# Optimization experiments

Hardware: AMD Instinct MI355X
Metric: run time of the kernel (lower is better)

Reference implementation:

```python
import jax, jax.numpy as jnp
import numpy as np

K = 3        # kernel_size
PAD = 1      # padding ('same' for stride 1)
RANK = 53    # CP rank from compression=10: round(27*32*64/(10*(9+32+64)))


def _kaiming_uniform(key, shape, fan_in):
    # matches nn.init.kaiming_uniform_(a=sqrt(5)): bound = 1/sqrt(fan_in)
    bound = 1.0 / np.sqrt(fan_in)
    return jax.random.uniform(key, shape, jnp.float32, -bound, bound)


def setup_inputs() -> dict:
    key = jax.random.key(0)
    ks = jax.random.split(key, 7)
    B, Cin, Cout, H, W, D = 1, 32, 64, 56, 56, 56
    x = jax.random.normal(ks[0], (B, Cin, H, W, D), jnp.float32)
    # CP factor matrices (fan_in = second dim for torch's 2D kaiming)
    U_kh = _kaiming_uniform(ks[1], (K, RANK), RANK)
    U_kw = _kaiming_uniform(ks[2], (K, RANK), RANK)
    U_kd = _kaiming_uniform(ks[3], (K, RANK), RANK)
    U_cin = _kaiming_uniform(ks[4], (Cin, RANK), RANK)
    U_cout = _kaiming_uniform(ks[5], (RANK, Cout), Cout)
    bias = jax.random.normal(ks[6], (Cout,), jnp.float32)
    return {"x": x, "U_kh": U_kh, "U_kw": U_kw, "U_kd": U_kd,
            "U_cin": U_cin, "U_cout": U_cout, "bias": bias}


def reference(x, U_kh, U_kw, U_kd, U_cin, U_cout, bias):
    B, C, H, W, D = x.shape
    xp = jnp.pad(x, ((0, 0), (0, 0), (PAD, PAD), (PAD, PAD), (PAD, PAD)))
    # im2col patches: patches[i,j,l,b,c,x,y,z] = xp[b,c,x+i,y+j,z+l]
    # (same values/ordering as torch unfold(2).unfold(3).unfold(4), stride=1)
    patches = jnp.stack([
        xp[:, :, i:i + H, j:j + W, l:l + D]
        for i in range(K) for j in range(K) for l in range(K)
    ]).reshape(K, K, K, B, C, H, W, D)
    # CP tensor-network contraction (legs: k_h,k_w,k_d,c_in share rank r -> c_out)
    out = jnp.einsum('ijlbcxyz,ir,jr,lr,cr,ro->boxyz',
                     patches, U_kh, U_kw, U_kd, U_cin, U_cout,
                     optimize=True)
    return out + bias[None, :, None, None, None]
```

## Files before the change

### kernel.cpp

```cpp
#include <hip/hip_runtime.h>


#define NP 175616
#define NQ 43904
#define HSTR 3136
#define QH 784
#define CIN 32
#define RK 53
#define COUT 64
#define SCR 53

__global__ __launch_bounds__(256) void k0_t(const float* __restrict__ Ucin,
                                            float* __restrict__ Ut)
{
    int t = blockIdx.x * 256 + threadIdx.x;
    if (t < RK * CIN) {
        int r = t >> 5, c = t & 31;
        Ut[t] = Ucin[c * RK + r];
    }
}

__global__ __launch_bounds__(256) void k1n(
    const float* __restrict__ x, const float* __restrict__ Ut,
    float* __restrict__ T1)
{
    const int p = blockIdx.x * 256 + threadIdx.x;
    float xv[CIN];
#pragma unroll
    for (int c = 0; c < CIN; ++c) xv[c] = x[c * NP + p];
#pragma unroll 2
    for (int r = 0; r < RK; ++r) {
        const float* U = Ut + r * CIN;
        float acc = 0.f;
#pragma unroll
        for (int c = 0; c < CIN; ++c) acc += xv[c] * U[c];
        T1[(size_t)r * NP + p] = acc;
    }
}

__global__ __launch_bounds__(256) void k2n(
    float* T1, const float* __restrict__ Ukw, const float* __restrict__ Ukd)
{
    __shared__ float sIn[3136];
    __shared__ float sA[3136];
    const int h = blockIdx.x;
    const int r = blockIdx.y;
    const int tid = threadIdx.x;
    const float kd0 = Ukd[r], kd1 = Ukd[RK + r], kd2 = Ukd[2 * RK + r];
    const float kw0 = Ukw[r], kw1 = Ukw[RK + r], kw2 = Ukw[2 * RK + r];
    float4* P4 = (float4*)(T1 + (size_t)r * NP + h * HSTR);

    for (int i = tid; i < QH; i += 256)
        ((float4*)sIn)[i] = P4[i];
    __syncthreads();

    for (int i = tid; i < QH; i += 256) {
        int w = i / 14, d0 = (i - w * 14) * 4;
        const float* b = &sIn[w * 56 + d0];
        float4 c = *(const float4*)b;
        float lm = (d0 > 0)  ? b[-1] : 0.f;
        float rp = (d0 < 52) ? b[4]  : 0.f;
        float4 o;
        o.x = lm  * kd0 + c.x * kd1 + c.y * kd2;
        o.y = c.x * kd0 + c.y * kd1 + c.z * kd2;
        o.z = c.y * kd0 + c.z * kd1 + c.w * kd2;
        o.w = c.z * kd0 + c.w * kd1 + rp  * kd2;
        ((float4*)sA)[i] = o;
    }
    __syncthreads();

    for (int i = tid; i < QH; i += 256) {
        int w = i / 14;
        float4 m = ((const float4*)sA)[i];
        float4 a0, a2;
        a0.x = a0.y = a0.z = a0.w = 0.f; a2 = a0;
        if (w > 0)  a0 = ((const float4*)sA)[i - 14];
        if (w < 55) a2 = ((const float4*)sA)[i + 14];
        float4 res;
        res.x = a0.x * kw0 + m.x * kw1 + a2.x * kw2;
        res.y = a0.y * kw0 + m.y * kw1 + a2.y * kw2;
        res.z = a0.z * kw0 + m.z * kw1 + a2.z * kw2;
        res.w = a0.w * kw0 + m.w * kw1 + a2.w * kw2;
        P4[i] = res;
    }
}

__global__ __launch_bounds__(256, 4) void k3n(
    const float4* __restrict__ Ta, const float* __restrict__ Ucout,
    const float* __restrict__ bias, const float* __restrict__ Ukh,
    float4* __restrict__ Out)
{
    const int lane = threadIdx.x & 63;
    int og = (threadIdx.x >> 6) << 4;
    og = __builtin_amdgcn_readfirstlane(og);
    const int q = blockIdx.x * 64 + lane;
    const int h = q / QH;
    const bool hm = (h > 0), hp = (h < 55);

    float4 a[16];
#pragma unroll
    for (int o = 0; o < 16; ++o) {
        float b = bias[og + o];
        a[o].x = b; a[o].y = b; a[o].z = b; a[o].w = b;
    }
#pragma unroll 2
    for (int r = 0; r < RK; ++r) {
        const float4* S = Ta + (size_t)r * NQ + q;
        const float k0 = Ukh[r], k1 = Ukh[RK + r], k2 = Ukh[2 * RK + r];
        float4 B = S[0];
        float4 A; A.x = 0.f; A.y = 0.f; A.z = 0.f; A.w = 0.f;
        float4 C = A;
        if (hm) A = S[-QH];
        if (hp) C = S[QH];
        float4 t;
        t.x = A.x * k0 + B.x * k1 + C.x * k2;
        t.y = A.y * k0 + B.y * k1 + C.y * k2;
        t.z = A.z * k0 + B.z * k1 + C.z * k2;
        t.w = A.w * k0 + B.w * k1 + C.w * k2;
        const float* Ur = Ucout + r * COUT + og;
#pragma unroll
        for (int o = 0; o < 16; ++o) {
            float u = Ur[o];
            a[o].x += t.x * u; a[o].y += t.y * u;
            a[o].z += t.z * u; a[o].w += t.w * u;
        }
    }
#pragma unroll
    for (int o = 0; o < 16; ++o)
        Out[(size_t)(og + o) * NQ + q] = a[o];
}


__global__ __launch_bounds__(256) void k1_chunk(
    const float* __restrict__ x, const float* __restrict__ Ucin,
    float* T, int r0, int nr)
{
    __shared__ float sU[11 * CIN];
    const int tid = threadIdx.x;
    for (int t = tid; t < nr * CIN; t += 256) {
        int lr = t >> 5, c = t & 31;
        sU[t] = Ucin[c * RK + (r0 + lr)];
    }
    __syncthreads();
    const int p = blockIdx.x * 256 + tid;
    float xv[CIN];
#pragma unroll
    for (int c = 0; c < CIN; ++c) xv[c] = x[c * NP + p];
#pragma unroll 1
    for (int lr = 0; lr < nr; ++lr) {
        float acc = 0.f;
#pragma unroll
        for (int c = 0; c < CIN; ++c) acc += xv[c] * sU[lr * CIN + c];
        T[(size_t)(SCR + lr) * NP + p] = acc;
    }
}

__global__ __launch_bounds__(256) void k2_chunk(
    const float* __restrict__ Ukh, const float* __restrict__ Ukw,
    const float* __restrict__ Ukd, float* T, int r0)
{
    __shared__ float sIn[5800];
    __shared__ float sA[5600];
    const int lr = blockIdx.z;
    const int r  = r0 + lr;
    const int h0 = blockIdx.x * 8, w0 = blockIdx.y * 8;
    const int tid = threadIdx.x;
    const float kh0 = Ukh[r], kh1 = Ukh[RK + r], kh2 = Ukh[2 * RK + r];
    const float kw0 = Ukw[r], kw1 = Ukw[RK + r], kw2 = Ukw[2 * RK + r];
    const float kd0 = Ukd[r], kd1 = Ukd[RK + r], kd2 = Ukd[2 * RK + r];
    const float* T1r = T + (size_t)(SCR + lr) * NP;

    for (int idx = tid; idx < 5800; idx += 256) {
        int d = idx % 58; int t2 = idx / 58; int ww = t2 % 10; int hh = t2 / 10;
        int gh = h0 + hh - 1, gw = w0 + ww - 1, gd = d - 1;
        float v = 0.f;
        if ((unsigned)gh < 56u && (unsigned)gw < 56u && (unsigned)gd < 56u)
            v = T1r[gh * HSTR + gw * 56 + gd];
        sIn[idx] = v;
    }
    __syncthreads();
    for (int idx = tid; idx < 5600; idx += 256) {
        int d = idx % 56; int t2 = idx / 56; int ww = t2 % 10; int hh = t2 / 10;
        const float* b = &sIn[(hh * 10 + ww) * 58 + d];
        sA[idx] = b[0] * kd0 + b[1] * kd1 + b[2] * kd2;
    }
    __syncthreads();
    const float k00 = kh0 * kw0, k01 = kh0 * kw1, k02 = kh0 * kw2;
    const float k10 = kh1 * kw0, k11 = kh1 * kw1, k12 = kh1 * kw2;
    const float k20 = kh2 * kw0, k21 = kh2 * kw1, k22 = kh2 * kw2;
    for (int idx = tid; idx < 3584; idx += 256) {
        int d = idx % 56; int t2 = idx / 56; int ww = t2 % 8; int hh = t2 / 8;
        const float* a = &sA[(hh * 10 + ww) * 56 + d];
        float acc = a[0]    * k00 + a[56]   * k01 + a[112]  * k02
                  + a[560]  * k10 + a[616]  * k11 + a[672]  * k12
                  + a[1120] * k20 + a[1176] * k21 + a[1232] * k22;
        T[(size_t)r * NP + (h0 + hh) * HSTR + (w0 + ww) * 56 + d] = acc;
    }
}

__global__ __launch_bounds__(256) void k3_out(
    float* T, const float* __restrict__ Ucout, const float* __restrict__ bias)
{
    __shared__ float sUo[RK * COUT];
    __shared__ float sB[COUT];
    const int tid = threadIdx.x;
    for (int t = tid; t < RK * COUT; t += 256) sUo[t] = Ucout[t];
    if (tid < COUT) sB[tid] = bias[tid];
    __syncthreads();
    const int p = blockIdx.x * 256 + tid;
    float acc[COUT];
#pragma unroll
    for (int o = 0; o < COUT; ++o) acc[o] = sB[o];
#pragma unroll 1
    for (int r = 0; r < RK; ++r) {
        float t = T[(size_t)r * NP + p];
        const float* Ur = &sUo[r * COUT];
#pragma unroll
        for (int o = 0; o < COUT; ++o) acc[o] += t * Ur[o];
    }
#pragma unroll
    for (int o = 0; o < COUT; ++o) T[(size_t)o * NP + p] = acc[o];
}


extern "C" void kernel_launch(void* const* d_in, const int* in_sizes, int n_in,
                              void* d_out, int out_size, void* d_ws, size_t ws_size,
                              hipStream_t stream)
{
    const float* x     = (const float*)d_in[0];
    const float* Ukh   = (const float*)d_in[1];
    const float* Ukw   = (const float*)d_in[2];
    const float* Ukd   = (const float*)d_in[3];
    const float* Ucin  = (const float*)d_in[4];
    const float* Ucout = (const float*)d_in[5];
    const float* bias  = (const float*)d_in[6];

    const size_t t1_bytes = (size_t)RK * NP * sizeof(float);

    if (ws_size >= t1_bytes + 8192) {
        float* T1 = (float*)d_ws;
        float* Ut = (float*)((char*)d_ws + t1_bytes);
        k0_t<<<7, 256, 0, stream>>>(Ucin, Ut);
        k1n<<<NP / 256, 256, 0, stream>>>(x, Ut, T1);
        k2n<<<dim3(56, RK), 256, 0, stream>>>(T1, Ukw, Ukd);
        k3n<<<NQ / 64, 256, 0, stream>>>((const float4*)T1, Ucout, bias, Ukh,
                                         (float4*)d_out);
    } else {
        float* T = (float*)d_out;
        for (int r0 = 0; r0 < RK; r0 += 11) {
            int nr = (RK - r0 < 11) ? (RK - r0) : 11;
            k1_chunk<<<NP / 256, 256, 0, stream>>>(x, Ucin, T, r0, nr);
            k2_chunk<<<dim3(7, 7, nr), 256, 0, stream>>>(Ukh, Ukw, Ukd, T, r0);
        }
        k3_out<<<NP / 256, 256, 0, stream>>>(T, Ucout, bias);
    }
}
```

Measured before the change: 173.2 us.

## Fuse depth-axis conv into rank projection and use float2 in output kernel

The depth-direction 3-tap filter moves into the Cin-to-rank projection kernel. Each wavefront holds one 56-wide depth row and exchanges neighbours with lane shuffles, so the width kernel needs only one shared buffer and one barrier. The final h-stencil and Cout kernel switches from float4 to float2 per thread, doubling the thread count for more parallelism. In exchange, 8 of every 64 lanes sit idle in the first kernel, and the output kernel now reads narrower vectors.

```diff
diff --git a/kernel.cpp b/kernel.cpp
--- a/kernel.cpp
+++ b/kernel.cpp
@@ -2,8 +2,9 @@
 
 
 #define NP 175616
-#define NQ 43904
+#define NP2 87808
 #define HSTR 3136
+#define H2 1568
 #define QH 784
 #define CIN 32
 #define RK 53
@@ -20,62 +21,55 @@
     }
 }
 
-__global__ __launch_bounds__(256) void k1n(
+__global__ __launch_bounds__(256) void k1d(
     const float* __restrict__ x, const float* __restrict__ Ut,
-    float* __restrict__ T1)
-{
-    const int p = blockIdx.x * 256 + threadIdx.x;
+    const float* __restrict__ Ukd, float* __restrict__ T1d)
+{
+    const int lane = threadIdx.x & 63;
+    const int row  = blockIdx.x * 4 + (threadIdx.x >> 6);
+    const int p    = row * 56 + lane;
+    const bool act = (lane < 56);
+
     float xv[CIN];
 #pragma unroll
-    for (int c = 0; c < CIN; ++c) xv[c] = x[c * NP + p];
+    for (int c = 0; c < CIN; ++c) xv[c] = act ? x[c * NP + p] : 0.f;
+
 #pragma unroll 2
     for (int r = 0; r < RK; ++r) {
         const float* U = Ut + r * CIN;
         float acc = 0.f;
 #pragma unroll
         for (int c = 0; c < CIN; ++c) acc += xv[c] * U[c];
-        T1[(size_t)r * NP + p] = acc;
-    }
-}
-
-__global__ __launch_bounds__(256) void k2n(
-    float* T1, const float* __restrict__ Ukw, const float* __restrict__ Ukd)
+        float lm = __shfl_up(acc, 1, 64);
+        float rp = __shfl_down(acc, 1, 64);
+        if (lane == 0)  lm = 0.f;
+        if (lane == 55) rp = 0.f;
+        float res = lm * Ukd[r] + acc * Ukd[RK + r] + rp * Ukd[2 * RK + r];
+        if (act) T1d[(size_t)r * NP + p] = res;
+    }
+}
+
+__global__ __launch_bounds__(256) void k2w(
+    float* T1d, const float* __restrict__ Ukw)
 {
     __shared__ float sIn[3136];
-    __shared__ float sA[3136];
     const int h = blockIdx.x;
     const int r = blockIdx.y;
     const int tid = threadIdx.x;
-    const float kd0 = Ukd[r], kd1 = Ukd[RK + r], kd2 = Ukd[2 * RK + r];
     const float kw0 = Ukw[r], kw1 = Ukw[RK + r], kw2 = Ukw[2 * RK + r];
-    float4* P4 = (float4*)(T1 + (size_t)r * NP + h * HSTR);
+    float4* P4 = (float4*)(T1d + (size_t)r * NP + h * HSTR);
 
     for (int i = tid; i < QH; i += 256)
         ((float4*)sIn)[i] = P4[i];
     __syncthreads();
 
     for (int i = tid; i < QH; i += 256) {
-        int w = i / 14, d0 = (i - w * 14) * 4;
-        const float* b = &sIn[w * 56 + d0];
-        float4 c = *(const float4*)b;
-        float lm = (d0 > 0)  ? b[-1] : 0.f;
-        float rp = (d0 < 52) ? b[4]  : 0.f;
-        float4 o;
-        o.x = lm  * kd0 + c.x * kd1 + c.y * kd2;
-        o.y = c.x * kd0 + c.y * kd1 + c.z * kd2;
-        o.z = c.y * kd0 + c.z * kd1 + c.w * kd2;
-        o.w = c.z * kd0 + c.w * kd1 + rp  * kd2;
-        ((float4*)sA)[i] = o;
-    }
-    __syncthreads();
-
-    for (int i = tid; i < QH; i += 256) {
         int w = i / 14;
-        float4 m = ((const float4*)sA)[i];
+        float4 m = ((const float4*)sIn)[i];
         float4 a0, a2;
         a0.x = a0.y = a0.z = a0.w = 0.f; a2 = a0;
-        if (w > 0)  a0 = ((const float4*)sA)[i - 14];
-        if (w < 55) a2 = ((const float4*)sA)[i + 14];
+        if (w > 0)  a0 = ((const float4*)sIn)[i - 14];
+        if (w < 55) a2 = ((const float4*)sIn)[i + 14];
         float4 res;
         res.x = a0.x * kw0 + m.x * kw1 + a2.x * kw2;
         res.y = a0.y * kw0 + m.y * kw1 + a2.y * kw2;
@@ -85,49 +79,46 @@
     }
 }
 
-__global__ __launch_bounds__(256, 4) void k3n(
-    const float4* __restrict__ Ta, const float* __restrict__ Ucout,
+__global__ __launch_bounds__(256, 4) void k3f2(
+    const float2* __restrict__ Ta, const float* __restrict__ Ucout,
     const float* __restrict__ bias, const float* __restrict__ Ukh,
-    float4* __restrict__ Out)
+    float2* __restrict__ Out)
 {
     const int lane = threadIdx.x & 63;
     int og = (threadIdx.x >> 6) << 4;
     og = __builtin_amdgcn_readfirstlane(og);
     const int q = blockIdx.x * 64 + lane;
-    const int h = q / QH;
+    const int h = q / H2;
     const bool hm = (h > 0), hp = (h < 55);
 
-    float4 a[16];
+    float2 a[16];
 #pragma unroll
     for (int o = 0; o < 16; ++o) {
         float b = bias[og + o];
-        a[o].x = b; a[o].y = b; a[o].z = b; a[o].w = b;
+        a[o].x = b; a[o].y = b;
     }
 #pragma unroll 2
     for (int r = 0; r < RK; ++r) {
-        const float4* S = Ta + (size_t)r * NQ + q;
+        const float2* S = Ta + (size_t)r * NP2 + q;
         const float k0 = Ukh[r], k1 = Ukh[RK + r], k2 = Ukh[2 * RK + r];
-        float4 B = S[0];
-        float4 A; A.x = 0.f; A.y = 0.f; A.z = 0.f; A.w = 0.f;
-        float4 C = A;
-        if (hm) A = S[-QH];
-        if (hp) C = S[QH];
-        float4 t;
+        float2 B = S[0];
+        float2 A; A.x = 0.f; A.y = 0.f;
+        float2 C = A;
+        if (hm) A = S[-H2];
+        if (hp) C = S[H2];
+        float2 t;
         t.x = A.x * k0 + B.x * k1 + C.x * k2;
         t.y = A.y * k0 + B.y * k1 + C.y * k2;
-        t.z = A.z * k0 + B.z * k1 + C.z * k2;
-        t.w = A.w * k0 + B.w * k1 + C.w * k2;
         const float* Ur = Ucout + r * COUT + og;
 #pragma unroll
         for (int o = 0; o < 16; ++o) {
             float u = Ur[o];
             a[o].x += t.x * u; a[o].y += t.y * u;
-            a[o].z += t.z * u; a[o].w += t.w * u;
         }
     }
 #pragma unroll
     for (int o = 0; o < 16; ++o)
-        Out[(size_t)(og + o) * NQ + q] = a[o];
+        Out[(size_t)(og + o) * NP2 + q] = a[o];
 }
 
 
@@ -241,10 +232,10 @@
         float* T1 = (float*)d_ws;
         float* Ut = (float*)((char*)d_ws + t1_bytes);
         k0_t<<<7, 256, 0, stream>>>(Ucin, Ut);
-        k1n<<<NP / 256, 256, 0, stream>>>(x, Ut, T1);
-        k2n<<<dim3(56, RK), 256, 0, stream>>>(T1, Ukw, Ukd);
-        k3n<<<NQ / 64, 256, 0, stream>>>((const float4*)T1, Ucout, bias, Ukh,
-                                         (float4*)d_out);
+        k1d<<<HSTR / 4, 256, 0, stream>>>(x, Ut, Ukd, T1);
+        k2w<<<dim3(56, RK), 256, 0, stream>>>(T1, Ukw);
+        k3f2<<<NP2 / 64, 256, 0, stream>>>((const float2*)T1, Ucout, bias, Ukh,
+                                           (float2*)d_out);
     } else {
         float* T = (float*)d_out;
         for (int r0 = 0; r0 < RK; r0 += 11) {
```

After: 159.2 us. 1.09x faster.
